# Kernel tuning notes

Measured on AMD Instinct MI355X. Metric: run time of the kernel, lower is better.

## Reference

```python
import jax, jax.numpy as jnp
import numpy as np

B, C, H, W = 32, 256, 32, 32
D = max(16, C // 4)  # 64
K = 8


def setup_inputs() -> dict:
    key = jax.random.key(0)
    ks = jax.random.split(key, 4)
    x = jax.random.normal(ks[0], (B, C, H, W), dtype=jnp.float32)
    wq = jax.random.normal(ks[1], (D, C), dtype=jnp.float32) * (1.0 / np.sqrt(C))
    wk = jax.random.normal(ks[2], (D, C), dtype=jnp.float32) * (1.0 / np.sqrt(C))
    wv = jax.random.normal(ks[3], (C, C), dtype=jnp.float32) * (1.0 / np.sqrt(C))
    bq = jnp.zeros((D,), dtype=jnp.float32)
    bk = jnp.zeros((D,), dtype=jnp.float32)
    bv = jnp.zeros((C,), dtype=jnp.float32)
    scale = jnp.ones((1,), dtype=jnp.float32)
    return {"x": x, "wq": wq, "bq": bq, "wk": wk, "bk": bk, "wv": wv, "bv": bv, "scale": scale}


def reference(x, wq, bq, wk, bk, wv, bv, scale):
    b, c, h, w = x.shape
    n = h * w
    xf = x.reshape(b, c, n)                      # [B,C,N]
    # 1x1 convs are pointwise GEMMs over the channel dim
    q = jnp.einsum('dc,bcn->bdn', wq, xf) + bq[None, :, None]   # [B,D,N]
    k = jnp.einsum('dc,bcn->bdn', wk, xf) + bk[None, :, None]   # [B,D,N]
    v = jnp.einsum('ec,bcn->ben', wv, xf) + bv[None, :, None]   # [B,C,N]
    d = q.shape[1]
    sim = jnp.einsum('bdn,bdm->bnm', q, k) / jnp.sqrt(jnp.float32(d))  # [B,N,N]
    sim = sim - 1e9 * jnp.eye(n, dtype=sim.dtype)[None]          # mask self
    topk_val, topk_idx = jax.lax.top_k(sim, K)                    # [B,N,K]
    weights = jax.nn.softmax(topk_val, axis=-1)                   # [B,N,K]
    v_t = v.transpose(0, 2, 1)                                    # [B,N,C]
    gathered = v_t[jnp.arange(b)[:, None, None], topk_idx]        # [B,N,K,C]
    out = jnp.einsum('bnk,bnkc->bnc', weights, gathered)          # [B,N,C]
    out = out.transpose(0, 2, 1).reshape(b, c, h, w)
    return x + scale * out
```

## Files before the change

kernel.cpp:

```cpp
#include <hip/hip_runtime.h>
#include <hip/hip_bf16.h>

#define B_ 32
#define C_ 256
#define N_ 1024
#define D_ 64

typedef __attribute__((ext_vector_type(8))) short bf16x8;
typedef __attribute__((ext_vector_type(4))) float f32x4;

__device__ __forceinline__ unsigned long long pack_key(float v, int m) {
    const unsigned int bits = __float_as_uint(v);
    const unsigned int mono = (bits & 0x80000000u) ? ~bits : (bits | 0x80000000u);
    return ((unsigned long long)mono << 10) | (unsigned long long)(1023 - m);
}

template <int CTRL>
__device__ __forceinline__ float dpp_mov_f(float x) {
    return __int_as_float(__builtin_amdgcn_update_dpp(
        0, __float_as_int(x), CTRL, 0xF, 0xF, true));
}
#define DPP_QUAD_XOR1   0xB1
#define DPP_QUAD_XOR2   0x4E
#define DPP_HALF_MIRROR 0x141
#define DPP_ROW_ROR8    0x128

template <int CTRL>
__device__ __forceinline__ unsigned long long dpp_max_u64(unsigned long long k) {
    const unsigned int lo = (unsigned int)k;
    const unsigned int hi = (unsigned int)(k >> 32);
    const unsigned int plo = (unsigned int)__builtin_amdgcn_update_dpp(0, (int)lo, CTRL, 0xF, 0xF, true);
    const unsigned int phi = (unsigned int)__builtin_amdgcn_update_dpp(0, (int)hi, CTRL, 0xF, 0xF, true);
    const unsigned long long p = ((unsigned long long)phi << 32) | plo;
    return p > k ? p : k;
}

__device__ __forceinline__ unsigned short f2bf(float f) {
    __hip_bfloat16 h = __float2bfloat16(f);
    return *(unsigned short*)&h;
}

__global__ __launch_bounds__(384) void wt_kernel(
    const float* __restrict__ wq, const float* __restrict__ wk,
    const float* __restrict__ wv, float* __restrict__ wt,
    unsigned short* __restrict__ wvb, int do_wvb)
{
    const int c = blockIdx.x;
    const int r = threadIdx.x;
    float v;
    if      (r < 64)  v = wq[(size_t)r * C_ + c];
    else if (r < 128) v = wk[(size_t)(r - 64) * C_ + c];
    else              v = wv[(size_t)(r - 128) * C_ + c];
    wt[(size_t)c * 384 + r] = v;
    if (do_wvb && r >= 128) {
        const int e = c, cc = r - 128;
        wvb[(size_t)e * C_ + cc] = f2bf(wv[(size_t)e * C_ + cc]);
    }
}

__global__ __launch_bounds__(256) void xt_kernel(
    const float* __restrict__ x, unsigned short* __restrict__ xtb)
{
    const int lid = blockIdx.x;
    const int b     = (lid & 7) + 8 * (lid >> 9);
    const int inner = (lid >> 3) & 63;
    const int nt    = inner & 15;
    const int ct    = inner >> 4;
    const int n0 = nt * 64, c0 = ct * 64;
    const int t  = threadIdx.x;

    __shared__ __align__(16) float tl[64][65];

    const float* xb = x + (size_t)b * C_ * N_;
    #pragma unroll
    for (int p = 0; p < 4; ++p) {
        const int cl = (t >> 4) + p * 16;
        const int nl = (t & 15) * 4;
        *(float4*)&tl[cl][nl] = *(const float4*)&xb[(size_t)(c0 + cl) * N_ + n0 + nl];
    }
    __syncthreads();

    unsigned short* dstb = xtb + ((size_t)b * N_) * C_;
    #pragma unroll
    for (int p = 0; p < 4; ++p) {
        const int nl = (t >> 4) + p * 16;
        const int cl = (t & 15) * 4;
        ushort4 o;
        o.x = f2bf(tl[cl + 0][nl]);
        o.y = f2bf(tl[cl + 1][nl]);
        o.z = f2bf(tl[cl + 2][nl]);
        o.w = f2bf(tl[cl + 3][nl]);
        *(ushort4*)&dstb[(size_t)(n0 + nl) * C_ + c0 + cl] = o;
    }
}

__global__ __launch_bounds__(256) void projqk_kernel(
    const float* __restrict__ x, const float* __restrict__ wt,
    const float* __restrict__ bq, const float* __restrict__ bk,
    float* __restrict__ qk)
{
    const int lid = blockIdx.x;
    const int b     = (lid & 7) + 8 * (lid >> 8);
    const int inner = (lid >> 3) & 31;
    const int rg    = inner & 7;
    const int nt    = inner >> 3;
    const int r0 = rg * 16;
    const int n0 = nt * 256;
    const int lane = threadIdx.x & 63;
    const int wu = __builtin_amdgcn_readfirstlane(threadIdx.x >> 6);
    const int rw = r0 + wu * 4;

    float acc[4][4];
    #pragma unroll
    for (int i = 0; i < 4; ++i)
        #pragma unroll
        for (int j = 0; j < 4; ++j) acc[i][j] = 0.f;

    const float* xp = x + (size_t)b * C_ * N_ + n0 + lane * 4;
    const float* wp = wt + rw;

    #pragma unroll 8
    for (int c = 0; c < C_; ++c) {
        const float4 xv = *(const float4*)(xp + (size_t)c * N_);
        const float4 w0 = *(const float4*)(wp + (size_t)c * 384);
        const float wv4[4] = { w0.x, w0.y, w0.z, w0.w };
        #pragma unroll
        for (int i = 0; i < 4; ++i) {
            acc[i][0] = fmaf(wv4[i], xv.x, acc[i][0]);
            acc[i][1] = fmaf(wv4[i], xv.y, acc[i][1]);
            acc[i][2] = fmaf(wv4[i], xv.z, acc[i][2]);
            acc[i][3] = fmaf(wv4[i], xv.w, acc[i][3]);
        }
    }

    #pragma unroll
    for (int i = 0; i < 4; ++i) {
        const int R = rw + i;
        const float bb = (R < 64) ? bq[R] : bk[R - 64];
        float4 o; o.x = acc[i][0]+bb; o.y = acc[i][1]+bb; o.z = acc[i][2]+bb; o.w = acc[i][3]+bb;
        *(float4*)&qk[((size_t)b * 128 + R) * N_ + n0 + lane * 4] = o;
    }
}

__global__ __launch_bounds__(256) void vmfma_kernel(
    const unsigned short* __restrict__ xtb, const unsigned short* __restrict__ wvb,
    const float* __restrict__ bv, float* __restrict__ vt)
{
    const int lid = blockIdx.x;
    const int b     = (lid & 7) + 8 * (lid >> 9);
    const int inner = (lid >> 3) & 63;
    const int nb    = inner & 15;
    const int eb    = inner >> 4;
    const int t  = threadIdx.x;
    const int lane = t & 63;
    const int w  = t >> 6;
    const int n_base = nb * 64 + (w & 1) * 32;
    const int e_base = eb * 64 + (w >> 1) * 32;

    const int l16  = lane & 15;
    const int koff = 8 * (lane >> 4);

    f32x4 acc[2][2];
    #pragma unroll
    for (int i = 0; i < 2; ++i)
        #pragma unroll
        for (int j = 0; j < 2; ++j) acc[i][j] = (f32x4)(0.f);

    const unsigned short* ab = wvb + (size_t)(e_base + l16) * C_ + koff;
    const unsigned short* bb = xtb + ((size_t)b * N_ + n_base + l16) * C_ + koff;

    #pragma unroll
    for (int kk = 0; kk < 8; ++kk) {
        const int c0 = kk * 32;
        bf16x8 a0 = *(const bf16x8*)(ab + c0);
        bf16x8 a1 = *(const bf16x8*)(ab + 16 * C_ + c0);
        bf16x8 b0 = *(const bf16x8*)(bb + c0);
        bf16x8 b1 = *(const bf16x8*)(bb + 16 * C_ + c0);
        acc[0][0] = __builtin_amdgcn_mfma_f32_16x16x32_bf16(a0, b0, acc[0][0], 0, 0, 0);
        acc[0][1] = __builtin_amdgcn_mfma_f32_16x16x32_bf16(a0, b1, acc[0][1], 0, 0, 0);
        acc[1][0] = __builtin_amdgcn_mfma_f32_16x16x32_bf16(a1, b0, acc[1][0], 0, 0, 0);
        acc[1][1] = __builtin_amdgcn_mfma_f32_16x16x32_bf16(a1, b1, acc[1][1], 0, 0, 0);
    }

    const int col  = lane & 15;
    const int row0 = (lane >> 4) * 4;
    #pragma unroll
    for (int i = 0; i < 2; ++i) {
        const int e0 = e_base + i * 16 + row0;
        const float4 bvv = *(const float4*)&bv[e0];
        #pragma unroll
        for (int j = 0; j < 2; ++j) {
            const int n = n_base + j * 16 + col;
            float4 o;
            o.x = acc[i][j][0] + bvv.x; o.y = acc[i][j][1] + bvv.y;
            o.z = acc[i][j][2] + bvv.z; o.w = acc[i][j][3] + bvv.w;
            *(float4*)&vt[((size_t)b * N_ + n) * C_ + e0] = o;
        }
    }
}

__global__ __launch_bounds__(256) void proj_full_kernel(
    const float* __restrict__ x, const float* __restrict__ wt,
    const float* __restrict__ bq, const float* __restrict__ bk,
    const float* __restrict__ bv,
    float* __restrict__ qk, float* __restrict__ vt)
{
    const int lid = blockIdx.x;
    const int b     = (lid & 7) + 8 * (lid / 384);
    const int inner = (lid >> 3) % 48;
    const int rg    = inner % 12;
    const int nt    = inner / 12;
    const int r0 = rg * 32;
    const int n0 = nt * 256;
    const int lane = threadIdx.x & 63;
    const int wu = __builtin_amdgcn_readfirstlane(threadIdx.x >> 6);
    const int rw = r0 + wu * 8;

    float acc[8][4];
    #pragma unroll
    for (int i = 0; i < 8; ++i)
        #pragma unroll
        for (int j = 0; j < 4; ++j) acc[i][j] = 0.f;

    const float* xp = x + (size_t)b * C_ * N_ + n0 + lane * 4;
    const float* wp = wt + rw;

    #pragma unroll 8
    for (int c = 0; c < C_; ++c) {
        const float4 xv = *(const float4*)(xp + (size_t)c * N_);
        const float* wr = wp + (size_t)c * 384;
        const float4 w0 = *(const float4*)(wr);
        const float4 w1 = *(const float4*)(wr + 4);
        const float wv8[8] = { w0.x, w0.y, w0.z, w0.w, w1.x, w1.y, w1.z, w1.w };
        #pragma unroll
        for (int i = 0; i < 8; ++i) {
            acc[i][0] = fmaf(wv8[i], xv.x, acc[i][0]);
            acc[i][1] = fmaf(wv8[i], xv.y, acc[i][1]);
            acc[i][2] = fmaf(wv8[i], xv.z, acc[i][2]);
            acc[i][3] = fmaf(wv8[i], xv.w, acc[i][3]);
        }
    }

    if (r0 < 128) {
        #pragma unroll
        for (int i = 0; i < 8; ++i) {
            const int R = rw + i;
            const float bb = (R < 64) ? bq[R] : bk[R - 64];
            float4 o; o.x = acc[i][0]+bb; o.y = acc[i][1]+bb; o.z = acc[i][2]+bb; o.w = acc[i][3]+bb;
            *(float4*)&qk[((size_t)b * 128 + R) * N_ + n0 + lane * 4] = o;
        }
    } else {
        const int e0 = rw - 128;
        float be[8];
        #pragma unroll
        for (int i = 0; i < 8; ++i) be[i] = bv[e0 + i];
        #pragma unroll
        for (int j = 0; j < 4; ++j) {
            const int n = n0 + lane * 4 + j;
            float* dst = &vt[((size_t)b * N_ + n) * C_ + e0];
            float4 o0; o0.x = acc[0][j]+be[0]; o0.y = acc[1][j]+be[1]; o0.z = acc[2][j]+be[2]; o0.w = acc[3][j]+be[3];
            float4 o1; o1.x = acc[4][j]+be[4]; o1.y = acc[5][j]+be[5]; o1.z = acc[6][j]+be[6]; o1.w = acc[7][j]+be[7];
            *(float4*)dst       = o0;
            *(float4*)(dst + 4) = o1;
        }
    }
}

__global__ __launch_bounds__(512) void attn_kernel(
    const float* __restrict__ x,
    const float* __restrict__ qk,
    const float* __restrict__ vt,
    const float* __restrict__ scale,
    float* __restrict__ out)
{
    const int lid = blockIdx.x;
    const int b  = (lid & 7) + 8 * (lid >> 9);
    const int n0 = ((lid >> 3) & 63) * 16;
    const int t  = threadIdx.x;
    const int lane = t & 63;
    const int w  = t >> 6;
    const int ms = w & 3;
    const int rg = __builtin_amdgcn_readfirstlane(t >> 8);

    __shared__ unsigned long long cand[16][196];
    __shared__ int   ccnt[16][4];

    const int m_base = ms * 256 + lane * 4;

    float a0[8], a1[8], a2[8], a3[8];
    #pragma unroll
    for (int r = 0; r < 8; ++r) { a0[r]=0.f; a1[r]=0.f; a2[r]=0.f; a3[r]=0.f; }

    const float* kb = qk + ((size_t)b * 128 + 64) * N_ + m_base;
    const float* qb = qk + (size_t)b * 128 * N_ + n0 + rg * 8;

    #pragma unroll 2
    for (int d0 = 0; d0 < D_; d0 += 4) {
        const float4 k0 = *(const float4*)&kb[(size_t)(d0+0) * N_];
        const float4 k1 = *(const float4*)&kb[(size_t)(d0+1) * N_];
        const float4 k2 = *(const float4*)&kb[(size_t)(d0+2) * N_];
        const float4 k3 = *(const float4*)&kb[(size_t)(d0+3) * N_];

        float qs[4][8];
        #pragma unroll
        for (int dd = 0; dd < 4; ++dd) {
            #pragma unroll
            for (int rq = 0; rq < 2; ++rq) {
                const float4 qv = *(const float4*)&qb[(size_t)(d0 + dd) * N_ + rq * 4];
                qs[dd][rq*4+0] = qv.x; qs[dd][rq*4+1] = qv.y;
                qs[dd][rq*4+2] = qv.z; qs[dd][rq*4+3] = qv.w;
            }
        }

        #pragma unroll
        for (int r = 0; r < 8; ++r) {
            a0[r] = fmaf(qs[0][r], k0.x, a0[r]); a0[r] = fmaf(qs[1][r], k1.x, a0[r]);
            a0[r] = fmaf(qs[2][r], k2.x, a0[r]); a0[r] = fmaf(qs[3][r], k3.x, a0[r]);
            a1[r] = fmaf(qs[0][r], k0.y, a1[r]); a1[r] = fmaf(qs[1][r], k1.y, a1[r]);
            a1[r] = fmaf(qs[2][r], k2.y, a1[r]); a1[r] = fmaf(qs[3][r], k3.y, a1[r]);
            a2[r] = fmaf(qs[0][r], k0.z, a2[r]); a2[r] = fmaf(qs[1][r], k1.z, a2[r]);
            a2[r] = fmaf(qs[2][r], k2.z, a2[r]); a2[r] = fmaf(qs[3][r], k3.z, a2[r]);
            a3[r] = fmaf(qs[0][r], k0.w, a3[r]); a3[r] = fmaf(qs[1][r], k1.w, a3[r]);
            a3[r] = fmaf(qs[2][r], k2.w, a3[r]); a3[r] = fmaf(qs[3][r], k3.w, a3[r]);
        }
    }

    const unsigned long long lt = (1ull << lane) - 1ull;
    #pragma unroll
    for (int r = 0; r < 8; ++r) {
        const int ri = rg * 8 + r;
        const int nrow = n0 + ri;
        float t0 = a0[r], t1 = a1[r], t2 = a2[r], t3 = a3[r];
        const int dj = nrow - m_base;
        if      (dj == 0) t0 = -1.0e9f;
        else if (dj == 1) t1 = -1.0e9f;
        else if (dj == 2) t2 = -1.0e9f;
        else if (dj == 3) t3 = -1.0e9f;

        float lm = fmaxf(fmaxf(t0, t1), fmaxf(t2, t3));
        lm = fmaxf(lm, dpp_mov_f<DPP_QUAD_XOR1>(lm));
        lm = fmaxf(lm, dpp_mov_f<DPP_QUAD_XOR2>(lm));
        lm = fmaxf(lm, dpp_mov_f<DPP_HALF_MIRROR>(lm));
        float Th = fminf(lm, dpp_mov_f<DPP_ROW_ROR8>(lm));
        Th = fminf(Th, __shfl_xor(Th, 16));
        Th = fminf(Th, __shfl_xor(Th, 32));

        int cnt = 0;
        {
            const bool p = (t0 >= Th);
            const unsigned long long msk = __ballot(p);
            const int pos = cnt + (int)__popcll(msk & lt);
            if (p && pos < 48) cand[ri][ms * 49 + pos] = pack_key(t0, m_base + 0);
            cnt += (int)__popcll(msk);
        }
        {
            const bool p = (t1 >= Th);
            const unsigned long long msk = __ballot(p);
            const int pos = cnt + (int)__popcll(msk & lt);
            if (p && pos < 48) cand[ri][ms * 49 + pos] = pack_key(t1, m_base + 1);
            cnt += (int)__popcll(msk);
        }
        {
            const bool p = (t2 >= Th);
            const unsigned long long msk = __ballot(p);
            const int pos = cnt + (int)__popcll(msk & lt);
            if (p && pos < 48) cand[ri][ms * 49 + pos] = pack_key(t2, m_base + 2);
            cnt += (int)__popcll(msk);
        }
        {
            const bool p = (t3 >= Th);
            const unsigned long long msk = __ballot(p);
            const int pos = cnt + (int)__popcll(msk & lt);
            if (p && pos < 48) cand[ri][ms * 49 + pos] = pack_key(t3, m_base + 3);
            cnt += (int)__popcll(msk);
        }

        if (cnt > 48) {
            unsigned long long K0 = pack_key(t0, m_base + 0);
            unsigned long long K1 = pack_key(t1, m_base + 1);
            unsigned long long K2 = pack_key(t2, m_base + 2);
            unsigned long long K3 = pack_key(t3, m_base + 3);
            #pragma unroll 1
            for (int round = 0; round < 8; ++round) {
                unsigned long long kl = K0 > K1 ? K0 : K1;
                kl = K2 > kl ? K2 : kl;
                kl = K3 > kl ? K3 : kl;
                #pragma unroll
                for (int off = 32; off >= 1; off >>= 1) {
                    const unsigned long long ks = __shfl_xor(kl, off);
                    if (ks > kl) kl = ks;
                }
                if (lane == 0) cand[ri][ms * 49 + round] = kl;
                if      (K0 == kl) K0 = 0ull;
                else if (K1 == kl) K1 = 0ull;
                else if (K2 == kl) K2 = 0ull;
                else if (K3 == kl) K3 = 0ull;
            }
            cnt = 8;
        }
        if (lane == 0) ccnt[ri][ms] = cnt;
    }
    __syncthreads();

    {
        const int half = lane >> 5;
        const int r    = w * 2 + half;
        const int l5   = lane & 31;

        unsigned long long k[6];
        #pragma unroll
        for (int s = 0; s < 4; ++s)
            k[s] = (l5 < ccnt[r][s]) ? cand[r][s * 49 + l5] : 0ull;
        #pragma unroll
        for (int j = 0; j < 2; ++j) {
            const int g   = l5 + 32 * j;
            const int s   = g >> 4;
            const int pos = 32 + (g & 15);
            k[4 + j] = (pos < ccnt[r][s]) ? cand[r][s * 49 + pos] : 0ull;
        }

        #pragma unroll 1
        for (int round = 0; round < 8; ++round) {
            unsigned long long km = k[0];
            #pragma unroll
            for (int q = 1; q < 6; ++q) km = k[q] > km ? k[q] : km;
            km = dpp_max_u64<DPP_QUAD_XOR1>(km);
            km = dpp_max_u64<DPP_QUAD_XOR2>(km);
            km = dpp_max_u64<DPP_HALF_MIRROR>(km);
            km = dpp_max_u64<DPP_ROW_ROR8>(km);
            { const unsigned long long p = __shfl_xor(km, 16); km = p > km ? p : km; }
            if (l5 == 0) cand[r][188 + round] = km;
            #pragma unroll
            for (int q = 0; q < 6; ++q) if (k[q] == km) k[q] = 0ull;
        }
    }

    const float* vtb = vt + (size_t)b * N_ * C_;
    #pragma unroll 1
    for (int rr = 0; rr < 2; ++rr) {
        const int r = w * 2 + rr;
        float ev[8]; unsigned int mi[8];
        float S = 0.f, vmax = 0.f;
        #pragma unroll
        for (int j = 0; j < 8; ++j) {
            const unsigned long long km = cand[r][188 + j];
            const unsigned int mono = (unsigned int)(km >> 10);
            mi[j] = 1023u - ((unsigned int)km & 1023u);
            const unsigned int bits = (mono & 0x80000000u) ? (mono & 0x7FFFFFFFu) : ~mono;
            const float vraw = __uint_as_float(bits);
            if (j == 0) vmax = vraw;
            const float e = __expf((vraw - vmax) * 0.125f);
            S += e;
            ev[j] = e;
        }

        float4 o = make_float4(0.f, 0.f, 0.f, 0.f);
        #pragma unroll
        for (int j = 0; j < 8; ++j) {
            const float4 vv = *(const float4*)&vtb[(size_t)mi[j] * C_ + lane * 4];
            o.x += ev[j] * vv.x; o.y += ev[j] * vv.y;
            o.z += ev[j] * vv.z; o.w += ev[j] * vv.w;
        }
        const float inv = 1.f / S;
        float* orow = (float*)&cand[r][0];
        *(float4*)&orow[lane * 4] = make_float4(o.x*inv, o.y*inv, o.z*inv, o.w*inv);
    }
    __syncthreads();

    const float sc = scale[0];
    const float* xb = x + (size_t)b * C_ * N_;
    float* ob = out + (size_t)b * C_ * N_;
    const int nl = t & 15;
    const int cg = t >> 4;
    const float* orow = (const float*)&cand[nl][0];
    #pragma unroll
    for (int i = 0; i < 8; ++i) {
        const int cc = i * 32 + cg;
        const size_t gi = (size_t)cc * N_ + n0 + nl;
        ob[gi] = xb[gi] + sc * orow[cc];
    }
}

extern "C" void kernel_launch(void* const* d_in, const int* in_sizes, int n_in,
                              void* d_out, int out_size, void* d_ws, size_t ws_size,
                              hipStream_t stream) {
    const float* x     = (const float*)d_in[0];
    const float* wq    = (const float*)d_in[1];
    const float* bq    = (const float*)d_in[2];
    const float* wk    = (const float*)d_in[3];
    const float* bk    = (const float*)d_in[4];
    const float* wv    = (const float*)d_in[5];
    const float* bv    = (const float*)d_in[6];
    const float* scale = (const float*)d_in[7];
    float* out = (float*)d_out;

    float* qk = (float*)d_ws;
    float* vt = qk + (size_t)B_ * 128 * N_;
    float* wt = vt + (size_t)B_ * N_ * C_;
    unsigned short* wvb = (unsigned short*)(wt + 256 * 384);
    unsigned short* xtb = wvb + (size_t)C_ * C_;

    const size_t needed = ((char*)(xtb + (size_t)B_ * N_ * C_)) - (char*)d_ws;
    const int mfma_path = (ws_size >= needed) ? 1 : 0;

    wt_kernel<<<dim3(256), 384, 0, stream>>>(wq, wk, wv, wt, wvb, mfma_path);
    if (mfma_path) {
        xt_kernel<<<dim3(2048), 256, 0, stream>>>(x, xtb);
        projqk_kernel<<<dim3(1024), 256, 0, stream>>>(x, wt, bq, bk, qk);
        vmfma_kernel<<<dim3(2048), 256, 0, stream>>>(xtb, wvb, bv, vt);
    } else {
        proj_full_kernel<<<dim3(1536), 256, 0, stream>>>(x, wt, bq, bk, bv, qk, vt);
    }
    attn_kernel<<<dim3(2048), 512, 0, stream>>>(x, qk, vt, scale, out);
}
```

Before: 178.0 us.

## Merge prep and projection launches and use packed FP32 FMA in GEMM loops

Combines the weight-transpose and x-transpose kernels into one launch, and the QK projection and V MFMA kernels into a second launch that dispatches on block index. This removes two kernel launches and the gaps between them. The QK projection and the attention similarity loop now use inline-asm v_pk_fma_f32 with an SGPR operand and op_sel, so each instruction performs two FMAs. The risk is that the "s" constraint forces a per-lane VGPR value into scalar registers, which may add readfirstlane or moves or be invalid if the Q/W values are not wave-uniform. Merging kernels also gives both paths the register footprint of the larger one.

```diff
diff --git a/kernel.cpp b/kernel.cpp
--- a/kernel.cpp
+++ b/kernel.cpp
@@ -35,41 +35,54 @@
     return p > k ? p : k;
 }
 
+template <int OS>
+__device__ __forceinline__ float2 pkb(float2 qp, float2 k, float2 a) {
+    float2 d;
+    if (OS == 0)
+        asm("v_pk_fma_f32 %0, %1, %2, %3 op_sel:[0,0,0] op_sel_hi:[0,1,1]"
+            : "=v"(d) : "s"(qp), "v"(k), "v"(a));
+    else
+        asm("v_pk_fma_f32 %0, %1, %2, %3 op_sel:[1,0,0] op_sel_hi:[1,1,1]"
+            : "=v"(d) : "s"(qp), "v"(k), "v"(a));
+    return d;
+}
+
 __device__ __forceinline__ unsigned short f2bf(float f) {
     __hip_bfloat16 h = __float2bfloat16(f);
     return *(unsigned short*)&h;
 }
 
-__global__ __launch_bounds__(384) void wt_kernel(
+__global__ __launch_bounds__(256) void prep_kernel(
+    const float* __restrict__ x,
     const float* __restrict__ wq, const float* __restrict__ wk,
     const float* __restrict__ wv, float* __restrict__ wt,
-    unsigned short* __restrict__ wvb, int do_wvb)
+    unsigned short* __restrict__ wvb, unsigned short* __restrict__ xtb,
+    int mfma_path)
 {
-    const int c = blockIdx.x;
-    const int r = threadIdx.x;
-    float v;
-    if      (r < 64)  v = wq[(size_t)r * C_ + c];
-    else if (r < 128) v = wk[(size_t)(r - 64) * C_ + c];
-    else              v = wv[(size_t)(r - 128) * C_ + c];
-    wt[(size_t)c * 384 + r] = v;
-    if (do_wvb && r >= 128) {
-        const int e = c, cc = r - 128;
-        wvb[(size_t)e * C_ + cc] = f2bf(wv[(size_t)e * C_ + cc]);
-    }
-}
-
-__global__ __launch_bounds__(256) void xt_kernel(
-    const float* __restrict__ x, unsigned short* __restrict__ xtb)
-{
-    const int lid = blockIdx.x;
+    __shared__ __align__(16) float tl[64][65];
+    const int bid = blockIdx.x;
+    const int t = threadIdx.x;
+
+    if (bid < 256) {
+        const int c = bid;
+        for (int r = t; r < 384; r += 256) {
+            float v;
+            if      (r < 64)  v = wq[(size_t)r * C_ + c];
+            else if (r < 128) v = wk[(size_t)(r - 64) * C_ + c];
+            else              v = wv[(size_t)(r - 128) * C_ + c];
+            wt[(size_t)c * 384 + r] = v;
+        }
+        if (mfma_path) wvb[(size_t)c * C_ + t] = f2bf(wv[(size_t)c * C_ + t]);
+        return;
+    }
+    if (!mfma_path) return;
+
+    const int lid = bid - 256;
     const int b     = (lid & 7) + 8 * (lid >> 9);
     const int inner = (lid >> 3) & 63;
     const int nt    = inner & 15;
     const int ct    = inner >> 4;
     const int n0 = nt * 64, c0 = ct * 64;
-    const int t  = threadIdx.x;
-
-    __shared__ __align__(16) float tl[64][65];
 
     const float* xb = x + (size_t)b * C_ * N_;
     #pragma unroll
@@ -94,107 +107,109 @@
     }
 }
 
-__global__ __launch_bounds__(256) void projqk_kernel(
+__global__ __launch_bounds__(256) void proj_kernel(
     const float* __restrict__ x, const float* __restrict__ wt,
     const float* __restrict__ bq, const float* __restrict__ bk,
-    float* __restrict__ qk)
-{
-    const int lid = blockIdx.x;
-    const int b     = (lid & 7) + 8 * (lid >> 8);
-    const int inner = (lid >> 3) & 31;
-    const int rg    = inner & 7;
-    const int nt    = inner >> 3;
-    const int r0 = rg * 16;
-    const int n0 = nt * 256;
-    const int lane = threadIdx.x & 63;
-    const int wu = __builtin_amdgcn_readfirstlane(threadIdx.x >> 6);
-    const int rw = r0 + wu * 4;
-
-    float acc[4][4];
-    #pragma unroll
-    for (int i = 0; i < 4; ++i)
-        #pragma unroll
-        for (int j = 0; j < 4; ++j) acc[i][j] = 0.f;
-
-    const float* xp = x + (size_t)b * C_ * N_ + n0 + lane * 4;
-    const float* wp = wt + rw;
-
-    #pragma unroll 8
-    for (int c = 0; c < C_; ++c) {
-        const float4 xv = *(const float4*)(xp + (size_t)c * N_);
-        const float4 w0 = *(const float4*)(wp + (size_t)c * 384);
-        const float wv4[4] = { w0.x, w0.y, w0.z, w0.w };
-        #pragma unroll
-        for (int i = 0; i < 4; ++i) {
-            acc[i][0] = fmaf(wv4[i], xv.x, acc[i][0]);
-            acc[i][1] = fmaf(wv4[i], xv.y, acc[i][1]);
-            acc[i][2] = fmaf(wv4[i], xv.z, acc[i][2]);
-            acc[i][3] = fmaf(wv4[i], xv.w, acc[i][3]);
-        }
-    }
-
-    #pragma unroll
-    for (int i = 0; i < 4; ++i) {
-        const int R = rw + i;
-        const float bb = (R < 64) ? bq[R] : bk[R - 64];
-        float4 o; o.x = acc[i][0]+bb; o.y = acc[i][1]+bb; o.z = acc[i][2]+bb; o.w = acc[i][3]+bb;
-        *(float4*)&qk[((size_t)b * 128 + R) * N_ + n0 + lane * 4] = o;
-    }
-}
-
-__global__ __launch_bounds__(256) void vmfma_kernel(
+    float* __restrict__ qk,
     const unsigned short* __restrict__ xtb, const unsigned short* __restrict__ wvb,
     const float* __restrict__ bv, float* __restrict__ vt)
 {
-    const int lid = blockIdx.x;
-    const int b     = (lid & 7) + 8 * (lid >> 9);
-    const int inner = (lid >> 3) & 63;
-    const int nb    = inner & 15;
-    const int eb    = inner >> 4;
-    const int t  = threadIdx.x;
+    const int bid = blockIdx.x;
+    const int t = threadIdx.x;
     const int lane = t & 63;
-    const int w  = t >> 6;
-    const int n_base = nb * 64 + (w & 1) * 32;
-    const int e_base = eb * 64 + (w >> 1) * 32;
-
-    const int l16  = lane & 15;
-    const int koff = 8 * (lane >> 4);
-
-    f32x4 acc[2][2];
-    #pragma unroll
-    for (int i = 0; i < 2; ++i)
-        #pragma unroll
-        for (int j = 0; j < 2; ++j) acc[i][j] = (f32x4)(0.f);
-
-    const unsigned short* ab = wvb + (size_t)(e_base + l16) * C_ + koff;
-    const unsigned short* bb = xtb + ((size_t)b * N_ + n_base + l16) * C_ + koff;
-
-    #pragma unroll
-    for (int kk = 0; kk < 8; ++kk) {
-        const int c0 = kk * 32;
-        bf16x8 a0 = *(const bf16x8*)(ab + c0);
-        bf16x8 a1 = *(const bf16x8*)(ab + 16 * C_ + c0);
-        bf16x8 b0 = *(const bf16x8*)(bb + c0);
-        bf16x8 b1 = *(const bf16x8*)(bb + 16 * C_ + c0);
-        acc[0][0] = __builtin_amdgcn_mfma_f32_16x16x32_bf16(a0, b0, acc[0][0], 0, 0, 0);
-        acc[0][1] = __builtin_amdgcn_mfma_f32_16x16x32_bf16(a0, b1, acc[0][1], 0, 0, 0);
-        acc[1][0] = __builtin_amdgcn_mfma_f32_16x16x32_bf16(a1, b0, acc[1][0], 0, 0, 0);
-        acc[1][1] = __builtin_amdgcn_mfma_f32_16x16x32_bf16(a1, b1, acc[1][1], 0, 0, 0);
-    }
-
-    const int col  = lane & 15;
-    const int row0 = (lane >> 4) * 4;
-    #pragma unroll
-    for (int i = 0; i < 2; ++i) {
-        const int e0 = e_base + i * 16 + row0;
-        const float4 bvv = *(const float4*)&bv[e0];
-        #pragma unroll
-        for (int j = 0; j < 2; ++j) {
-            const int n = n_base + j * 16 + col;
+
+    if (bid < 1024) {
+        const int lid = bid;
+        const int b     = (lid & 7) + 8 * (lid >> 8);
+        const int inner = (lid >> 3) & 31;
+        const int rg    = inner & 7;
+        const int nt    = inner >> 3;
+        const int r0 = rg * 16;
+        const int n0 = nt * 256;
+        const int wu = __builtin_amdgcn_readfirstlane(t >> 6);
+        const int rw = r0 + wu * 4;
+
+        float2 acc2[4][2];
+        #pragma unroll
+        for (int i = 0; i < 4; ++i) {
+            acc2[i][0] = make_float2(0.f, 0.f);
+            acc2[i][1] = make_float2(0.f, 0.f);
+        }
+
+        const float* xp = x + (size_t)b * C_ * N_ + n0 + lane * 4;
+        const float* wp = wt + rw;
+
+        #pragma unroll 8
+        for (int c = 0; c < C_; ++c) {
+            const float2 x01 = *(const float2*)(xp + (size_t)c * N_);
+            const float2 x23 = *(const float2*)(xp + (size_t)c * N_ + 2);
+            const float4 w4 = *(const float4*)(wp + (size_t)c * 384);
+            float2 wA; wA.x = w4.x; wA.y = w4.y;
+            float2 wB; wB.x = w4.z; wB.y = w4.w;
+            acc2[0][0] = pkb<0>(wA, x01, acc2[0][0]); acc2[0][1] = pkb<0>(wA, x23, acc2[0][1]);
+            acc2[1][0] = pkb<1>(wA, x01, acc2[1][0]); acc2[1][1] = pkb<1>(wA, x23, acc2[1][1]);
+            acc2[2][0] = pkb<0>(wB, x01, acc2[2][0]); acc2[2][1] = pkb<0>(wB, x23, acc2[2][1]);
+            acc2[3][0] = pkb<1>(wB, x01, acc2[3][0]); acc2[3][1] = pkb<1>(wB, x23, acc2[3][1]);
+        }
+
+        #pragma unroll
+        for (int i = 0; i < 4; ++i) {
+            const int R = rw + i;
+            const float bb = (R < 64) ? bq[R] : bk[R - 64];
             float4 o;
-            o.x = acc[i][j][0] + bvv.x; o.y = acc[i][j][1] + bvv.y;
-            o.z = acc[i][j][2] + bvv.z; o.w = acc[i][j][3] + bvv.w;
-            *(float4*)&vt[((size_t)b * N_ + n) * C_ + e0] = o;
+            o.x = acc2[i][0].x + bb; o.y = acc2[i][0].y + bb;
+            o.z = acc2[i][1].x + bb; o.w = acc2[i][1].y + bb;
+            *(float4*)&qk[((size_t)b * 128 + R) * N_ + n0 + lane * 4] = o;
+        }
+    } else {
+        const int lid = bid - 1024;
+        const int b     = (lid & 7) + 8 * (lid >> 9);
+        const int inner = (lid >> 3) & 63;
+        const int nb    = inner & 15;
+        const int eb    = inner >> 4;
+        const int w  = t >> 6;
+        const int n_base = nb * 64 + (w & 1) * 32;
+        const int e_base = eb * 64 + (w >> 1) * 32;
+
+        const int l16  = lane & 15;
+        const int koff = 8 * (lane >> 4);
+
+        f32x4 acc[2][2];
+        #pragma unroll
+        for (int i = 0; i < 2; ++i)
+            #pragma unroll
+            for (int j = 0; j < 2; ++j) acc[i][j] = (f32x4)(0.f);
+
+        const unsigned short* ab = wvb + (size_t)(e_base + l16) * C_ + koff;
+        const unsigned short* bb = xtb + ((size_t)b * N_ + n_base + l16) * C_ + koff;
+
+        #pragma unroll
+        for (int kk = 0; kk < 8; ++kk) {
+            const int c0 = kk * 32;
+            bf16x8 a0 = *(const bf16x8*)(ab + c0);
+            bf16x8 a1 = *(const bf16x8*)(ab + 16 * C_ + c0);
+            bf16x8 b0 = *(const bf16x8*)(bb + c0);
+            bf16x8 b1 = *(const bf16x8*)(bb + 16 * C_ + c0);
+            acc[0][0] = __builtin_amdgcn_mfma_f32_16x16x32_bf16(a0, b0, acc[0][0], 0, 0, 0);
+            acc[0][1] = __builtin_amdgcn_mfma_f32_16x16x32_bf16(a0, b1, acc[0][1], 0, 0, 0);
+            acc[1][0] = __builtin_amdgcn_mfma_f32_16x16x32_bf16(a1, b0, acc[1][0], 0, 0, 0);
+            acc[1][1] = __builtin_amdgcn_mfma_f32_16x16x32_bf16(a1, b1, acc[1][1], 0, 0, 0);
+        }
+
+        const int col  = lane & 15;
+        const int row0 = (lane >> 4) * 4;
+        #pragma unroll
+        for (int i = 0; i < 2; ++i) {
+            const int e0 = e_base + i * 16 + row0;
+            const float4 bvv = *(const float4*)&bv[e0];
+            #pragma unroll
+            for (int j = 0; j < 2; ++j) {
+                const int n = n_base + j * 16 + col;
+                float4 o;
+                o.x = acc[i][j][0] + bvv.x; o.y = acc[i][j][1] + bvv.y;
+                o.z = acc[i][j][2] + bvv.z; o.w = acc[i][j][3] + bvv.w;
+                *(float4*)&vt[((size_t)b * N_ + n) * C_ + e0] = o;
+            }
         }
     }
 }
@@ -287,41 +302,40 @@
 
     const int m_base = ms * 256 + lane * 4;
 
-    float a0[8], a1[8], a2[8], a3[8];
+    float2 A01[8], A23[8];
     #pragma unroll
-    for (int r = 0; r < 8; ++r) { a0[r]=0.f; a1[r]=0.f; a2[r]=0.f; a3[r]=0.f; }
+    for (int r = 0; r < 8; ++r) {
+        A01[r] = make_float2(0.f, 0.f);
+        A23[r] = make_float2(0.f, 0.f);
+    }
 
     const float* kb = qk + ((size_t)b * 128 + 64) * N_ + m_base;
     const float* qb = qk + (size_t)b * 128 * N_ + n0 + rg * 8;
 
     #pragma unroll 2
     for (int d0 = 0; d0 < D_; d0 += 4) {
-        const float4 k0 = *(const float4*)&kb[(size_t)(d0+0) * N_];
-        const float4 k1 = *(const float4*)&kb[(size_t)(d0+1) * N_];
-        const float4 k2 = *(const float4*)&kb[(size_t)(d0+2) * N_];
-        const float4 k3 = *(const float4*)&kb[(size_t)(d0+3) * N_];
-
-        float qs[4][8];
+        float2 k01[4], k23[4];
         #pragma unroll
         for (int dd = 0; dd < 4; ++dd) {
-            #pragma unroll
-            for (int rq = 0; rq < 2; ++rq) {
-                const float4 qv = *(const float4*)&qb[(size_t)(d0 + dd) * N_ + rq * 4];
-                qs[dd][rq*4+0] = qv.x; qs[dd][rq*4+1] = qv.y;
-                qs[dd][rq*4+2] = qv.z; qs[dd][rq*4+3] = qv.w;
-            }
-        }
-
-        #pragma unroll
-        for (int r = 0; r < 8; ++r) {
-            a0[r] = fmaf(qs[0][r], k0.x, a0[r]); a0[r] = fmaf(qs[1][r], k1.x, a0[r]);
-            a0[r] = fmaf(qs[2][r], k2.x, a0[r]); a0[r] = fmaf(qs[3][r], k3.x, a0[r]);
-            a1[r] = fmaf(qs[0][r], k0.y, a1[r]); a1[r] = fmaf(qs[1][r], k1.y, a1[r]);
-            a1[r] = fmaf(qs[2][r], k2.y, a1[r]); a1[r] = fmaf(qs[3][r], k3.y, a1[r]);
-            a2[r] = fmaf(qs[0][r], k0.z, a2[r]); a2[r] = fmaf(qs[1][r], k1.z, a2[r]);
-            a2[r] = fmaf(qs[2][r], k2.z, a2[r]); a2[r] = fmaf(qs[3][r], k3.z, a2[r]);
-            a3[r] = fmaf(qs[0][r], k0.w, a3[r]); a3[r] = fmaf(qs[1][r], k1.w, a3[r]);
-            a3[r] = fmaf(qs[2][r], k2.w, a3[r]); a3[r] = fmaf(qs[3][r], k3.w, a3[r]);
+            k01[dd] = *(const float2*)&kb[(size_t)(d0+dd) * N_];
+            k23[dd] = *(const float2*)&kb[(size_t)(d0+dd) * N_ + 2];
+        }
+        #pragma unroll
+        for (int dd = 0; dd < 4; ++dd) {
+            const float4 qv0 = *(const float4*)&qb[(size_t)(d0+dd) * N_ + 0];
+            const float4 qv1 = *(const float4*)&qb[(size_t)(d0+dd) * N_ + 4];
+            float2 qpA; qpA.x = qv0.x; qpA.y = qv0.y;
+            float2 qpB; qpB.x = qv0.z; qpB.y = qv0.w;
+            float2 qpC; qpC.x = qv1.x; qpC.y = qv1.y;
+            float2 qpD; qpD.x = qv1.z; qpD.y = qv1.w;
+            A01[0] = pkb<0>(qpA, k01[dd], A01[0]); A23[0] = pkb<0>(qpA, k23[dd], A23[0]);
+            A01[1] = pkb<1>(qpA, k01[dd], A01[1]); A23[1] = pkb<1>(qpA, k23[dd], A23[1]);
+            A01[2] = pkb<0>(qpB, k01[dd], A01[2]); A23[2] = pkb<0>(qpB, k23[dd], A23[2]);
+            A01[3] = pkb<1>(qpB, k01[dd], A01[3]); A23[3] = pkb<1>(qpB, k23[dd], A23[3]);
+            A01[4] = pkb<0>(qpC, k01[dd], A01[4]); A23[4] = pkb<0>(qpC, k23[dd], A23[4]);
+            A01[5] = pkb<1>(qpC, k01[dd], A01[5]); A23[5] = pkb<1>(qpC, k23[dd], A23[5]);
+            A01[6] = pkb<0>(qpD, k01[dd], A01[6]); A23[6] = pkb<0>(qpD, k23[dd], A23[6]);
+            A01[7] = pkb<1>(qpD, k01[dd], A01[7]); A23[7] = pkb<1>(qpD, k23[dd], A23[7]);
         }
     }
 
@@ -330,7 +344,7 @@
     for (int r = 0; r < 8; ++r) {
         const int ri = rg * 8 + r;
         const int nrow = n0 + ri;
-        float t0 = a0[r], t1 = a1[r], t2 = a2[r], t3 = a3[r];
+        float t0 = A01[r].x, t1 = A01[r].y, t2 = A23[r].x, t3 = A23[r].y;
         const int dj = nrow - m_base;
         if      (dj == 0) t0 = -1.0e9f;
         else if (dj == 1) t1 = -1.0e9f;
@@ -503,11 +517,9 @@
     const size_t needed = ((char*)(xtb + (size_t)B_ * N_ * C_)) - (char*)d_ws;
     const int mfma_path = (ws_size >= needed) ? 1 : 0;
 
-    wt_kernel<<<dim3(256), 384, 0, stream>>>(wq, wk, wv, wt, wvb, mfma_path);
+    prep_kernel<<<dim3(256 + 2048), 256, 0, stream>>>(x, wq, wk, wv, wt, wvb, xtb, mfma_path);
     if (mfma_path) {
-        xt_kernel<<<dim3(2048), 256, 0, stream>>>(x, xtb);
-        projqk_kernel<<<dim3(1024), 256, 0, stream>>>(x, wt, bq, bk, qk);
-        vmfma_kernel<<<dim3(2048), 256, 0, stream>>>(xtb, wvb, bv, vt);
+        proj_kernel<<<dim3(1024 + 2048), 256, 0, stream>>>(x, wt, bq, bk, qk, xtb, wvb, bv, vt);
     } else {
         proj_full_kernel<<<dim3(1536), 256, 0, stream>>>(x, wt, bq, bk, bv, qk, vt);
     }
```

Result: slower. 237.1 us (+33.2%).
